# Kernel optimization log

Hardware: AMD Instinct MI355X
Metric: run time of the kernel (lower is better)

The kernel has to match this reference:

```python
import jax, jax.numpy as jnp
import numpy as np

H = 2048          # hidden_size
NH = 16           # num_heads
HD = H // NH      # head_dim = 128
B, S = 2, 2048


def setup_inputs() -> dict:
    key = jax.random.key(0)
    ks = jax.random.split(key, 9)
    sc_h = 1.0 / np.sqrt(H)
    x = jax.random.normal(ks[0], (B, S, H), dtype=jnp.float32)
    # torch nn.Linear weights are [out_features, in_features]
    Wq = jax.random.uniform(ks[1], (H, H), jnp.float32, -sc_h, sc_h)
    bq = jax.random.uniform(ks[2], (H,), jnp.float32, -sc_h, sc_h)
    Wk = jax.random.uniform(ks[3], (HD, H), jnp.float32, -sc_h, sc_h)
    bk = jax.random.uniform(ks[4], (HD,), jnp.float32, -sc_h, sc_h)
    Wv = jax.random.uniform(ks[5], (HD, H), jnp.float32, -sc_h, sc_h)
    bv = jax.random.uniform(ks[6], (HD,), jnp.float32, -sc_h, sc_h)
    Wo = jax.random.uniform(ks[7], (H, H), jnp.float32, -sc_h, sc_h)
    bo = jax.random.uniform(ks[8], (H,), jnp.float32, -sc_h, sc_h)
    return {"x": x, "Wq": Wq, "bq": bq, "Wk": Wk, "bk": bk,
            "Wv": Wv, "bv": bv, "Wo": Wo, "bo": bo}


def reference(x, Wq, bq, Wk, bk, Wv, bv, Wo, bo):
    b, s, _ = x.shape
    q = (jnp.einsum('bsh,oh->bso', x, Wq) + bq).reshape(b, s, NH, HD)
    q = q.transpose(0, 2, 1, 3)                      # [b, nh, s, hd]
    k = jnp.einsum('bsh,dh->bsd', x, Wk) + bk        # [b, s, hd] single KV head
    v = jnp.einsum('bsh,dh->bsd', x, Wv) + bv
    # shared-K attention scores: broadcast single K head across query heads
    attn = jnp.einsum('bnsd,btd->bnst', q, k) / jnp.sqrt(jnp.float32(HD))
    attn = jax.nn.softmax(attn, axis=-1)
    out = jnp.einsum('bnst,btd->bnsd', attn, v)      # [b, nh, s, hd]
    out = out.transpose(0, 2, 1, 3).reshape(b, s, H)
    return jnp.einsum('bsh,oh->bso', out, Wo) + bo
```

## Files before the change

### kernel.cpp

```cpp
#include <hip/hip_runtime.h>
#include <hip/hip_bf16.h>

typedef unsigned short u16;
typedef __bf16 bf16x8 __attribute__((ext_vector_type(8)));
typedef float f32x4 __attribute__((ext_vector_type(4)));

#define AS1 __attribute__((address_space(1)))
#define AS3 __attribute__((address_space(3)))

__device__ __forceinline__ u16 f2bf(float f) {
  unsigned u = __builtin_bit_cast(unsigned, f);
  u += 0x7FFFu + ((u >> 16) & 1u);
  return (u16)(u >> 16);
}

__device__ __forceinline__ void gload_lds16(const void* g, void* l) {
  __builtin_amdgcn_global_load_lds((AS1 void*)g, (AS3 void*)l, 16, 0, 0);
}

__global__ __launch_bounds__(256) void cvt_bf16(const float* __restrict__ in,
                                                u16* __restrict__ out, int n,
                                                float scale) {
  int i = (blockIdx.x * 256 + threadIdx.x) * 8;
  if (i >= n) return;
  float4 a = *(const float4*)(in + i);
  float4 b = *(const float4*)(in + i + 4);
  u16 t[8] = {f2bf(a.x * scale), f2bf(a.y * scale), f2bf(a.z * scale), f2bf(a.w * scale),
              f2bf(b.x * scale), f2bf(b.y * scale), f2bf(b.z * scale), f2bf(b.w * scale)};
  *(uint4*)(out + i) = *(const uint4*)t;
}

__global__ __launch_bounds__(256)
void cvt_weights(const float* __restrict__ Wq, const float* __restrict__ Wk,
                 const float* __restrict__ Wv, const float* __restrict__ Wo,
                 u16* __restrict__ wqkv, u16* __restrict__ wo, float qs) {
  const long NQ = 524288, NK = 32768, NV = 32768;
  long i = (long)blockIdx.x * 256 + threadIdx.x;
  const float* src;
  u16* dst;
  float s = 1.f;
  if (i < NQ) { src = Wq + i * 8; dst = wqkv + i * 8; s = qs; }
  else if (i < NQ + NK) { long j = i - NQ; src = Wk + j * 8; dst = wqkv + 2048l * 2048 + j * 8; }
  else if (i < NQ + NK + NV) { long j = i - NQ - NK; src = Wv + j * 8; dst = wqkv + 2176l * 2048 + j * 8; }
  else { long j = i - NQ - NK - NV; src = Wo + j * 8; dst = wo + j * 8; }
  float4 a = *(const float4*)src;
  float4 b = *(const float4*)(src + 4);
  u16 t[8] = {f2bf(a.x * s), f2bf(a.y * s), f2bf(a.z * s), f2bf(a.w * s),
              f2bf(b.x * s), f2bf(b.y * s), f2bf(b.z * s), f2bf(b.w * s)};
  *(uint4*)dst = *(const uint4*)t;
}

__global__ void build_bias(const float* __restrict__ bq, const float* __restrict__ bk,
                           const float* __restrict__ bv, float* __restrict__ out,
                           float s) {
  int t = blockIdx.x * 256 + threadIdx.x;
  if (t < 2048) out[t] = bq[t] * s;
  else if (t < 2176) out[t] = bk[t - 2048];
  else if (t < 2304) out[t] = bv[t - 2176];
}

template<int MODE>
__global__ __launch_bounds__(256)
void gemm_bt(const u16* __restrict__ A, const u16* __restrict__ B,
             const float* __restrict__ bias, void* __restrict__ C0,
             void* __restrict__ C1, void* __restrict__ C2,
             int M, int N, int K, float scale)
{
  __shared__ u16 As[128 * 32];
  __shared__ u16 Bs[128 * 32];
  const int tid = threadIdx.x;
  const int wave = tid >> 6, lane = tid & 63;
  const int g = lane >> 4, r = lane & 15;
  const int wrow = (wave >> 1) * 64, wcol = (wave & 1) * 64;
  const long tM = (long)blockIdx.y * 128, tN = (long)blockIdx.x * 128;

  const int r0 = wave * 16 + (lane >> 2);
  const int c0 = (lane & 3) * 8;

  f32x4 acc[4][4] = {};
  char* As3 = (char*)As;
  char* Bs3 = (char*)Bs;

  for (int kt = 0; kt < K; kt += 32) {
    __syncthreads();
    const u16* gA = A + (tM + r0) * K + kt + c0;
    const u16* gB = B + (tN + r0) * K + kt + c0;
    gload_lds16(gA,                As3 + wave * 1024);
    gload_lds16(gA + (long)64 * K, As3 + 4096 + wave * 1024);
    gload_lds16(gB,                Bs3 + wave * 1024);
    gload_lds16(gB + (long)64 * K, Bs3 + 4096 + wave * 1024);
    __syncthreads();

    bf16x8 a[4], b[4];
#pragma unroll
    for (int m = 0; m < 4; m++)
      a[m] = *(const bf16x8*)(As + (wrow + m * 16 + r) * 32 + g * 8);
#pragma unroll
    for (int n = 0; n < 4; n++)
      b[n] = *(const bf16x8*)(Bs + (wcol + n * 16 + r) * 32 + g * 8);
#pragma unroll
    for (int m = 0; m < 4; m++)
#pragma unroll
      for (int n = 0; n < 4; n++)
        acc[m][n] = __builtin_amdgcn_mfma_f32_16x16x32_bf16(a[m], b[n], acc[m][n], 0, 0, 0);
  }

#pragma unroll
  for (int m = 0; m < 4; m++) {
    const long row0 = tM + wrow + m * 16 + g * 4;
#pragma unroll
    for (int n = 0; n < 4; n++) {
      const long col = tN + wcol + n * 16 + r;
      const float bb = bias[col];
      if (MODE == 0) {
#pragma unroll
        for (int q = 0; q < 4; q++)
          ((float*)C0)[(row0 + q) * N + col] = (acc[m][n][q] + bb) * scale;
      } else {
        u16 vals[4];
#pragma unroll
        for (int q = 0; q < 4; q++) vals[q] = f2bf(acc[m][n][q] + bb);
        if (col < 2048) {
#pragma unroll
          for (int q = 0; q < 4; q++)
            ((u16*)C0)[(row0 + q) * 2048 + col] = vals[q];
        } else if (col < 2176) {
#pragma unroll
          for (int q = 0; q < 4; q++)
            ((u16*)C1)[(row0 + q) * 128 + (col - 2048)] = vals[q];
        } else {
          const long b2 = row0 >> 11, t = row0 & 2047;
          *(ushort4*)((u16*)C2 + (b2 * 128 + (col - 2176)) * 2048 + t) =
              *(const ushort4*)vals;
        }
      }
    }
  }
}

__global__ __launch_bounds__(256, 2)
void attn_mqa10(const u16* __restrict__ Q, const u16* __restrict__ Kb,
                const u16* __restrict__ VT, u16* __restrict__ O)
{
  constexpr int S = 2048;
  const int bid = blockIdx.x;
  const int qt = bid & 15;
  const int head = (bid >> 4) & 15;
  const int b = bid >> 8;
  const int tid = threadIdx.x;
  const int wave = tid >> 6, lane = tid & 63;
  const int g = lane >> 4, r = lane & 15;

  __shared__ u16 Ks[2][64 * 128];
  __shared__ u16 VTs[2][128 * 64];
  __shared__ u16 Ps[4][16 * 72];

  bf16x8 qf[2][4];
#pragma unroll
  for (int qb = 0; qb < 2; qb++) {
    const u16* qp = Q + (long)(b * S + qt * 128 + qb * 64 + wave * 16 + r) * 2048
                      + head * 128 + g * 8;
#pragma unroll
    for (int ks = 0; ks < 4; ks++) qf[qb][ks] = *(const bf16x8*)(qp + ks * 32);
  }

  f32x4 oacc[2][8] = {};
  float lsum[2][4] = {};

  auto stageK = [&](int buf, int t0) {
    char* dst = (char*)Ks[buf];
#pragma unroll
    for (int p = 0; p < 4; p++) {
      int D = p * 4096 + wave * 1024 + lane * 16;
      int row = D >> 8;
      int col2 = (D & 255) ^ ((row & 7) << 4);
      gload_lds16(Kb + ((long)b * S + t0 + row) * 128 + (col2 >> 1), dst + D);
    }
  };
  auto stageV = [&](int buf, int t0) {
    char* dst = (char*)VTs[buf];
#pragma unroll
    for (int p = 0; p < 4; p++) {
      int D = p * 4096 + wave * 1024 + lane * 16;
      int row = D >> 7;
      int colb = (D & 127) ^ ((row & 7) << 4);
      gload_lds16(VT + ((long)b * 128 + row) * 2048 + t0 + (colb >> 1), dst + D);
    }
  };

  stageK(0, 0);
  stageV(0, 0);
  __syncthreads();

  for (int t0 = 0; t0 < S; t0 += 64) {
    const int cur = (t0 >> 6) & 1;
    const bool nxt = (t0 + 64) < S;

    if (nxt) { stageK(cur ^ 1, t0 + 64); stageV(cur ^ 1, t0 + 64); }

    char* Ks3 = (char*)Ks[cur];
    f32x4 st[2][4] = {};
#pragma unroll
    for (int ks = 0; ks < 4; ks++) {
#pragma unroll
      for (int nf = 0; nf < 4; nf++) {
        const int trow = nf * 16 + r;
        const int col2 = (ks * 64 + g * 16) ^ ((trow & 7) << 4);
        bf16x8 kf = *(const bf16x8*)(Ks3 + trow * 256 + col2);
        st[0][nf] = __builtin_amdgcn_mfma_f32_16x16x32_bf16(qf[0][ks], kf, st[0][nf], 0, 0, 0);
        st[1][nf] = __builtin_amdgcn_mfma_f32_16x16x32_bf16(qf[1][ks], kf, st[1][nf], 0, 0, 0);
      }
    }

    char* Vs3 = (char*)VTs[cur];
    bf16x8 vreg[2][8];
#pragma unroll
    for (int qb = 0; qb < 2; qb++) {
#pragma unroll
      for (int nf = 0; nf < 4; nf++) {
#pragma unroll
        for (int q = 0; q < 4; q++) {
          float p = exp2f(st[qb][nf][q]);
          lsum[qb][q] += p;
          Ps[wave][(g * 4 + q) * 72 + nf * 16 + r] =
              __builtin_bit_cast(u16, (__bf16)p);
        }
      }
#pragma unroll
      for (int ks = 0; ks < 2; ks++) {
        bf16x8 pf = *(const bf16x8*)(&Ps[wave][r * 72 + ks * 32 + g * 8]);
#pragma unroll
        for (int dn = 0; dn < 8; dn++) {
          if (qb == 0) {
            const int d = dn * 16 + r;
            vreg[ks][dn] = *(const bf16x8*)(Vs3 + d * 128 +
                                            ((ks * 64 + g * 16) ^ ((d & 7) << 4)));
          }
          oacc[qb][dn] = __builtin_amdgcn_mfma_f32_16x16x32_bf16(pf, vreg[ks][dn],
                                                                 oacc[qb][dn], 0, 0, 0);
        }
      }
    }

    __syncthreads();
  }

#pragma unroll
  for (int off = 1; off < 16; off <<= 1)
#pragma unroll
    for (int qb = 0; qb < 2; qb++)
#pragma unroll
      for (int q = 0; q < 4; q++)
        lsum[qb][q] += __shfl_xor(lsum[qb][q], off);

#pragma unroll
  for (int qb = 0; qb < 2; qb++) {
#pragma unroll
    for (int q = 0; q < 4; q++) {
      const float inv = 1.f / lsum[qb][q];
      const long orow = (long)(b * S + qt * 128 + qb * 64 + wave * 16 + g * 4 + q);
#pragma unroll
      for (int dn = 0; dn < 8; dn++)
        O[orow * 2048 + head * 128 + dn * 16 + r] = f2bf(oacc[qb][dn][q] * inv);
    }
  }
}

extern "C" void kernel_launch(void* const* d_in, const int* in_sizes, int n_in,
                              void* d_out, int out_size, void* d_ws, size_t ws_size,
                              hipStream_t stream) {
  const float* x  = (const float*)d_in[0];
  const float* Wq = (const float*)d_in[1];
  const float* bq = (const float*)d_in[2];
  const float* Wk = (const float*)d_in[3];
  const float* bk = (const float*)d_in[4];
  const float* Wv = (const float*)d_in[5];
  const float* bv = (const float*)d_in[6];
  const float* Wo = (const float*)d_in[7];
  const float* bo = (const float*)d_in[8];
  float* out = (float*)d_out;

  char* ws = (char*)d_ws;
  u16* x_bf     = (u16*)(ws + (0ul  << 20));
  u16* q_bf     = (u16*)(ws + (16ul << 20));
  u16* wqkv_bf  = (u16*)(ws + (32ul << 20));
  u16* wo_bf    = (u16*)(ws + (42ul << 20));
  u16* k_bf     = (u16*)(ws + (50ul << 20));
  u16* vt_bf    = (u16*)(ws + (51ul << 20));
  u16* attn_bf  = (u16*)(ws + (52ul << 20));
  float* bias_a = (float*)(ws + (68ul << 20));

  const int BS = 4096, H = 2048;
  const float QS = 0.12751744f;

  cvt_bf16<<<BS * H / 8 / 256, 256, 0, stream>>>(x, x_bf, BS * H, 1.f);
  cvt_weights<<<4352, 256, 0, stream>>>(Wq, Wk, Wv, Wo, wqkv_bf, wo_bf, QS);
  build_bias<<<9, 256, 0, stream>>>(bq, bk, bv, bias_a, QS);

  gemm_bt<3><<<dim3(18, 32), 256, 0, stream>>>(
      x_bf, wqkv_bf, bias_a, q_bf, k_bf, vt_bf, 4096, 2304, 2048, 1.0f);
  attn_mqa10<<<512, 256, 0, stream>>>(q_bf, k_bf, vt_bf, attn_bf);
  gemm_bt<0><<<dim3(16, 32), 256, 0, stream>>>(
      attn_bf, wo_bf, bo, out, nullptr, nullptr, 4096, 2048, 2048, 1.0f);
}
```

Before: 232.7 us.

## Permute V^T layout for vectorized swizzled P stores, remap GEMM blocks, fuse bias

The QKV GEMM now writes V^T with the token order permuted inside each 64-token chunk. Each lane's four P values for a row are therefore contiguous, so the attention kernel can store them to shared memory as one ushort4 with an XOR swizzle instead of four scalar stores to a padded buffer. The GEMM also remaps block indices so consecutive tiles go to the same XCD group, aiming at better L2 reuse. The bias-building kernel is folded into the weight-conversion kernel to remove one launch. The risk is that the swizzle and permutation have to line up exactly with how P and V are read as MFMA operands.

```diff
diff --git a/kernel.cpp b/kernel.cpp
--- a/kernel.cpp
+++ b/kernel.cpp
@@ -33,9 +33,20 @@
 __global__ __launch_bounds__(256)
 void cvt_weights(const float* __restrict__ Wq, const float* __restrict__ Wk,
                  const float* __restrict__ Wv, const float* __restrict__ Wo,
-                 u16* __restrict__ wqkv, u16* __restrict__ wo, float qs) {
-  const long NQ = 524288, NK = 32768, NV = 32768;
+                 const float* __restrict__ bq, const float* __restrict__ bk,
+                 const float* __restrict__ bv,
+                 u16* __restrict__ wqkv, u16* __restrict__ wo,
+                 float* __restrict__ bias_a, float qs) {
+  const long NQ = 524288, NK = 32768, NV = 32768, NO = 524288;
+  const long NW = NQ + NK + NV + NO;
   long i = (long)blockIdx.x * 256 + threadIdx.x;
+  if (i >= NW) {
+    int t = (int)(i - NW);
+    if (t < 2048) bias_a[t] = bq[t] * qs;
+    else if (t < 2176) bias_a[t] = bk[t - 2048];
+    else if (t < 2304) bias_a[t] = bv[t - 2176];
+    return;
+  }
   const float* src;
   u16* dst;
   float s = 1.f;
@@ -48,15 +59,6 @@
   u16 t[8] = {f2bf(a.x * s), f2bf(a.y * s), f2bf(a.z * s), f2bf(a.w * s),
               f2bf(b.x * s), f2bf(b.y * s), f2bf(b.z * s), f2bf(b.w * s)};
   *(uint4*)dst = *(const uint4*)t;
-}
-
-__global__ void build_bias(const float* __restrict__ bq, const float* __restrict__ bk,
-                           const float* __restrict__ bv, float* __restrict__ out,
-                           float s) {
-  int t = blockIdx.x * 256 + threadIdx.x;
-  if (t < 2048) out[t] = bq[t] * s;
-  else if (t < 2176) out[t] = bk[t - 2048];
-  else if (t < 2304) out[t] = bv[t - 2176];
 }
 
 template<int MODE>
@@ -72,7 +74,12 @@
   const int wave = tid >> 6, lane = tid & 63;
   const int g = lane >> 4, r = lane & 15;
   const int wrow = (wave >> 1) * 64, wcol = (wave & 1) * 64;
-  const long tM = (long)blockIdx.y * 128, tN = (long)blockIdx.x * 128;
+
+  const int gx = gridDim.x;
+  int lin = blockIdx.y * gx + blockIdx.x;
+  const int cpx = (gx * gridDim.y) >> 3;
+  lin = (lin & 7) * cpx + (lin >> 3);
+  const long tM = (long)(lin / gx) * 128, tN = (long)(lin % gx) * 128;
 
   const int r0 = wave * 16 + (lane >> 2);
   const int c0 = (lane & 3) * 8;
@@ -129,9 +136,14 @@
           for (int q = 0; q < 4; q++)
             ((u16*)C1)[(row0 + q) * 128 + (col - 2048)] = vals[q];
         } else {
-          const long b2 = row0 >> 11, t = row0 & 2047;
-          *(ushort4*)((u16*)C2 + (b2 * 128 + (col - 2176)) * 2048 + t) =
-              *(const ushort4*)vals;
+          const long b2 = row0 >> 11;
+          const long t0r = row0 & 2047;
+          const int tl = (int)(t0r & 63);
+          const int rbase = tl & 15, blk = tl >> 4;
+          u16* vp = (u16*)C2 + (b2 * 128 + (col - 2176)) * 2048 + (t0r >> 6) * 64;
+#pragma unroll
+          for (int q = 0; q < 4; q++)
+            vp[(rbase + q) * 4 + blk] = vals[q];
         }
       }
     }
@@ -139,7 +151,7 @@
 }
 
 __global__ __launch_bounds__(256, 2)
-void attn_mqa10(const u16* __restrict__ Q, const u16* __restrict__ Kb,
+void attn_mqa11(const u16* __restrict__ Q, const u16* __restrict__ Kb,
                 const u16* __restrict__ VT, u16* __restrict__ O)
 {
   constexpr int S = 2048;
@@ -153,7 +165,7 @@
 
   __shared__ u16 Ks[2][64 * 128];
   __shared__ u16 VTs[2][128 * 64];
-  __shared__ u16 Ps[4][16 * 72];
+  __shared__ u16 Ps[4][16 * 64];
 
   bf16x8 qf[2][4];
 #pragma unroll
@@ -166,6 +178,7 @@
 
   f32x4 oacc[2][8] = {};
   float lsum[2][4] = {};
+  char* psb = (char*)Ps[wave];
 
   auto stageK = [&](int buf, int t0) {
     char* dst = (char*)Ks[buf];
@@ -217,18 +230,22 @@
 #pragma unroll
     for (int qb = 0; qb < 2; qb++) {
 #pragma unroll
-      for (int nf = 0; nf < 4; nf++) {
-#pragma unroll
-        for (int q = 0; q < 4; q++) {
+      for (int q = 0; q < 4; q++) {
+        const int prow = g * 4 + q;
+        u16 pk[4];
+#pragma unroll
+        for (int nf = 0; nf < 4; nf++) {
           float p = exp2f(st[qb][nf][q]);
           lsum[qb][q] += p;
-          Ps[wave][(g * 4 + q) * 72 + nf * 16 + r] =
-              __builtin_bit_cast(u16, (__bf16)p);
+          pk[nf] = __builtin_bit_cast(u16, (__bf16)p);
         }
+        *(ushort4*)(psb + prow * 128 + ((r * 8) ^ ((prow & 7) << 4))) =
+            *(const ushort4*)pk;
       }
 #pragma unroll
       for (int ks = 0; ks < 2; ks++) {
-        bf16x8 pf = *(const bf16x8*)(&Ps[wave][r * 72 + ks * 32 + g * 8]);
+        bf16x8 pf = *(const bf16x8*)(psb + r * 128 +
+                                     ((ks * 64 + g * 16) ^ ((r & 7) << 4)));
 #pragma unroll
         for (int dn = 0; dn < 8; dn++) {
           if (qb == 0) {
@@ -294,12 +311,12 @@
   const float QS = 0.12751744f;
 
   cvt_bf16<<<BS * H / 8 / 256, 256, 0, stream>>>(x, x_bf, BS * H, 1.f);
-  cvt_weights<<<4352, 256, 0, stream>>>(Wq, Wk, Wv, Wo, wqkv_bf, wo_bf, QS);
-  build_bias<<<9, 256, 0, stream>>>(bq, bk, bv, bias_a, QS);
+  cvt_weights<<<4361, 256, 0, stream>>>(Wq, Wk, Wv, Wo, bq, bk, bv,
+                                        wqkv_bf, wo_bf, bias_a, QS);
 
   gemm_bt<3><<<dim3(18, 32), 256, 0, stream>>>(
       x_bf, wqkv_bf, bias_a, q_bf, k_bf, vt_bf, 4096, 2304, 2048, 1.0f);
-  attn_mqa10<<<512, 256, 0, stream>>>(q_bf, k_bf, vt_bf, attn_bf);
+  attn_mqa11<<<512, 256, 0, stream>>>(q_bf, k_bf, vt_bf, attn_bf);
   gemm_bt<0><<<dim3(16, 32), 256, 0, stream>>>(
       attn_bf, wo_bf, bo, out, nullptr, nullptr, 4096, 2048, 2048, 1.0f);
 }
```

Measured after the change: 224.5 us. 1.04x faster.
